# Kernel optimization log

Measured on AMD Instinct MI355X. Metric: run time of the kernel, lower is better.

Reference implementation:

```python
import jax, jax.numpy as jnp
import numpy as np

N_NODES = 131072      # total nodes across all graphs
IN_CHANNELS = 256     # node attribute dim after continuous WL embedding
NUM_PROJ = 256        # num_projections
NUM_QUANT = 256       # num_quantiles
NUM_GRAPHS = 256      # batch of graphs (equal-sized segments of 512 nodes)
P_NORM = 2            # p-sliced Wasserstein


def setup_inputs() -> dict:
    key = jax.random.key(0)
    k1, k2 = jax.random.split(key)
    x = jax.random.normal(k1, (N_NODES, IN_CHANNELS), dtype=jnp.float32)
    # fixed random projections, column-normalized (resample_projections)
    projections = jax.random.normal(k2, (IN_CHANNELS, NUM_PROJ), dtype=jnp.float32)
    projections = projections / jnp.sqrt(jnp.sum(projections ** 2, axis=0, keepdims=True))
    # cum_weights buffer: linspace(0, 1, num_quantiles)
    cum_weights = jnp.linspace(0.0, 1.0, NUM_QUANT, dtype=jnp.float32)
    # equal-sized graph segments (sorted segment ids), jit-friendly
    batch = (jnp.arange(N_NODES, dtype=jnp.int32) // (N_NODES // NUM_GRAPHS))
    return {
        "x": x,
        "projections": projections,
        "cum_weights": cum_weights,
        "batch": batch,
        "num_graphs": NUM_GRAPHS,
    }


def reference(x, projections, cum_weights, batch, num_graphs):
    # x: [N, C], projections: [C, P], cum_weights: [Q]
    n_nodes = x.shape[0]
    num_p = projections.shape[1]
    num_q = cum_weights.shape[0]
    nodes_per_graph = n_nodes // num_graphs

    xp = jnp.matmul(x, projections)                       # [N, P]
    xg = xp.reshape(num_graphs, nodes_per_graph, num_p)   # [B, n, P]
    xs = jnp.sort(xg, axis=1)                             # segmented sort per graph
    # torch.quantile(..., interpolation='lower'): index = floor(q * (n-1))
    idx = jnp.floor(cum_weights * (nodes_per_graph - 1)).astype(jnp.int32)  # [Q]
    quant = xs[:, idx, :]                                 # [B, Q, P]
    scale = (num_q * num_p) ** (1.0 / P_NORM)
    return quant.reshape(num_graphs, num_q * num_p) / scale
```

## Files before the change

kernel.cpp:

```cpp
#include <hip/hip_runtime.h>
#include <hip/hip_fp16.h>

typedef unsigned short u16;
typedef unsigned int u32;
typedef __bf16 bf16x8 __attribute__((ext_vector_type(8)));
typedef float f32x4 __attribute__((ext_vector_type(4)));


__device__ __forceinline__ u16 f2bf(float f) {
  union { float f; u32 u; } v; v.f = f;
  u32 r = (v.u + 0x7FFFu + ((v.u >> 16) & 1u)) >> 16;
  return (u16)r;
}

__device__ __forceinline__ u32 cvtpk(float a, float b) {
  u32 r; asm("v_cvt_pk_bf16_f32 %0, %1, %2" : "=v"(r) : "v"(a), "v"(b));
  return r;
}

__device__ __forceinline__ u32 pkh(float a, float b) {
  return (u32)__half_as_ushort(__float2half(a)) |
         ((u32)__half_as_ushort(__float2half(b)) << 16);
}

__device__ __forceinline__ u32 vperm(u32 s0, u32 s1, u32 sel) {
  u32 r; asm("v_perm_b32 %0, %1, %2, %3" : "=v"(r) : "v"(s0), "v"(s1), "s"(sel));
  return r;
}

__device__ __forceinline__ u32 pkmin(u32 a, u32 b) {
  u32 r; asm("v_pk_min_f16 %0, %1, %2" : "=v"(r) : "v"(a), "v"(b)); return r;
}
__device__ __forceinline__ u32 pkmax(u32 a, u32 b) {
  u32 r; asm("v_pk_max_f16 %0, %1, %2" : "=v"(r) : "v"(a), "v"(b)); return r;
}

template <int CTRL> __device__ __forceinline__ u32 xdpp(u32 x) {
  return (u32)__builtin_amdgcn_mov_dpp((int)x, CTRL, 0xF, 0xF, true);
}
template <int IMM> __device__ __forceinline__ u32 xswz(u32 x) {
  return (u32)__builtin_amdgcn_ds_swizzle((int)x, IMM);
}
#define EX_X1(x)  xdpp<0xB1>(x)
#define EX_X2(x)  xdpp<0x4E>(x)
#define EX_F3(x)  xdpp<0x1B>(x)
#define EX_F7(x)  xdpp<0x141>(x)
#define EX_F15(x) xdpp<0x140>(x)
#define EX_X8(x)  xdpp<0x128>(x)
#define EX_X4(x)  xswz<0x101F>(x)
#define EX_X16(x) xswz<0x401F>(x)
#define EX_F31(x) xswz<0x7C1F>(x)
#define EX_F63(x) ((u32)__shfl_xor((int)(x), 63, 64))

__global__ __launch_bounds__(256) void transpose_proj(const float* __restrict__ proj,
                                                      u16* __restrict__ projT) {
  const int k = blockIdx.x;
  const int p = threadIdx.x;
  projT[(size_t)p * 256 + k] = f2bf(proj[(size_t)k * 256 + p]);
}

__global__ __launch_bounds__(1024) void fused_swe(const float* __restrict__ x,
                                                  const u16* __restrict__ projT,
                                                  const float* __restrict__ cw,
                                                  float* __restrict__ out) {
  extern __shared__ __attribute__((aligned(16))) char lds[];
  u32* res = (u32*)(lds + 32768);

  const int tid = threadIdx.x;
  const int lane = tid & 63;
  const int w = tid >> 6;
  const int g = blockIdx.x;
  const int quad = lane >> 4;
  const int m16 = lane & 15;

  bf16x8 a[2][8];
#pragma unroll
  for (int t = 0; t < 2; ++t) {
    const float* ap = x + (size_t)(g * 512 + w * 32 + t * 16 + m16) * 256 + quad * 8;
#pragma unroll
    for (int ks = 0; ks < 8; ++ks) {
      float4 f0 = *(const float4*)(ap + ks * 32);
      float4 f1 = *(const float4*)(ap + ks * 32 + 4);
      u32 pk4[4] = { cvtpk(f0.x, f0.y), cvtpk(f0.z, f0.w),
                     cvtpk(f1.x, f1.y), cvtpk(f1.z, f1.w) };
      a[t][ks] = *(const bf16x8*)pk4;
    }
  }

  for (int qtr = 0; qtr < 4; ++qtr) {
    {
      const int row = tid >> 4;
      const int seg0 = tid & 15;
#pragma unroll
      for (int si = 0; si < 2; ++si) {
        const int seg = seg0 + si * 16;
        uint4 d = *(const uint4*)(projT + (size_t)(qtr * 64 + row) * 256 + seg * 8);
        *(uint4*)(lds + row * 512 + ((seg ^ (row & 7)) * 16)) = d;
      }
    }
    __syncthreads();

#pragma unroll
    for (int nt = 0; nt < 4; ++nt) {
      const int prow = nt * 16 + m16;
      const int rx = (prow & 7) << 4;
      const char* pb = lds + prow * 512;
      f32x4 acc0 = {0.f, 0.f, 0.f, 0.f};
      f32x4 acc1 = {0.f, 0.f, 0.f, 0.f};
#pragma unroll
      for (int ks = 0; ks < 8; ++ks) {
        bf16x8 bfrag = *(const bf16x8*)(pb + (((ks * 64) | (quad * 16)) ^ rx));
        acc0 = __builtin_amdgcn_mfma_f32_16x16x32_bf16(a[0][ks], bfrag, acc0, 0, 0, 0);
        acc1 = __builtin_amdgcn_mfma_f32_16x16x32_bf16(a[1][ks], bfrag, acc1, 0, 0, 0);
      }
      const int wb = prow * 260 + w * 16 + quad * 2;
      res[wb]     = pkh(acc0[0], acc0[1]);
      res[wb + 1] = pkh(acc0[2], acc0[3]);
      res[wb + 8] = pkh(acc1[0], acc1[1]);
      res[wb + 9] = pkh(acc1[2], acc1[3]);
    }
    __syncthreads();

#pragma unroll
    for (int s = 0; s < 2; ++s) {
      const int d = w * 2 + s;
      u32* ra = res + d * 260;
      u32* rb = res + (d + 32) * 260;
      uint4 a4 = *(const uint4*)(ra + lane * 4);
      uint4 b4 = *(const uint4*)(rb + lane * 4);
      u32 v[8];
      v[0] = vperm(b4.x, a4.x, 0x05040100u); v[1] = vperm(b4.x, a4.x, 0x07060302u);
      v[2] = vperm(b4.y, a4.y, 0x05040100u); v[3] = vperm(b4.y, a4.y, 0x07060302u);
      v[4] = vperm(b4.z, a4.z, 0x05040100u); v[5] = vperm(b4.z, a4.z, 0x07060302u);
      v[6] = vperm(b4.w, a4.w, 0x05040100u); v[7] = vperm(b4.w, a4.w, 0x07060302u);

#define CE(i, j) { u32 mn_ = pkmin(v[i], v[j]); u32 mx_ = pkmax(v[i], v[j]); v[i] = mn_; v[j] = mx_; }
#define INTRA3 \
  CE(0,4) CE(1,5) CE(2,6) CE(3,7) \
  CE(0,2) CE(1,3) CE(4,6) CE(5,7) \
  CE(0,1) CE(2,3) CE(4,5) CE(6,7)

#define FLIPP(EX, lowbit) { \
    const bool low_ = (lane & (lowbit)) == 0; \
    u32 t_[8]; \
    _Pragma("unroll") for (int r = 0; r < 8; ++r) t_[r] = EX(v[7 - r]); \
    _Pragma("unroll") for (int r = 0; r < 8; ++r) { \
      u32 mn_ = pkmin(v[r], t_[r]); u32 mx_ = pkmax(v[r], t_[r]); \
      v[r] = low_ ? mn_ : mx_; } }

#define XCROSSP(EX, lm) { \
    const bool low_ = (lane & (lm)) == 0; \
    _Pragma("unroll") for (int r = 0; r < 8; ++r) { \
      u32 t_ = EX(v[r]); \
      u32 mn_ = pkmin(v[r], t_); u32 mx_ = pkmax(v[r], t_); \
      v[r] = low_ ? mn_ : mx_; } }

      CE(0,1) CE(2,3) CE(4,5) CE(6,7)
      CE(0,3) CE(1,2) CE(4,7) CE(5,6)
      CE(0,1) CE(2,3) CE(4,5) CE(6,7)
      CE(0,7) CE(1,6) CE(2,5) CE(3,4)
      CE(0,2) CE(1,3) CE(4,6) CE(5,7)
      CE(0,1) CE(2,3) CE(4,5) CE(6,7)
      FLIPP(EX_X1, 1)  INTRA3
      FLIPP(EX_F3, 2)  XCROSSP(EX_X1, 1)  INTRA3
      FLIPP(EX_F7, 4)  XCROSSP(EX_X2, 2) XCROSSP(EX_X1, 1)  INTRA3
      FLIPP(EX_F15, 8) XCROSSP(EX_X4, 4) XCROSSP(EX_X2, 2) XCROSSP(EX_X1, 1)  INTRA3
      FLIPP(EX_F31, 16) XCROSSP(EX_X8, 8) XCROSSP(EX_X4, 4) XCROSSP(EX_X2, 2) XCROSSP(EX_X1, 1)  INTRA3
      FLIPP(EX_F63, 32) XCROSSP(EX_X16, 16) XCROSSP(EX_X8, 8) XCROSSP(EX_X4, 4) XCROSSP(EX_X2, 2) XCROSSP(EX_X1, 1)  INTRA3

#undef CE
#undef INTRA3
#undef FLIPP
#undef XCROSSP

      u32* pp = (lane < 32) ? (ra + lane * 8) : (rb + lane * 8 - 256);
      *(uint4*)pp       = (uint4){v[0], v[1], v[2], v[3]};
      *(uint4*)(pp + 4) = (uint4){v[4], v[5], v[6], v[7]};
    }
    __syncthreads();

#pragma unroll
    for (int it = 0; it < 16; ++it) {
      const int linear = it * 1024 + tid;
      const int q = linear >> 6;
      const int pc = linear & 63;
      const int iq = (int)floorf(cw[q] * 511.0f);
      const int dd = pc & 31;
      const u32 val = res[dd * 260 + ((iq >= 256) ? (iq + 8064) : iq)];
      const u16 h = (pc & 32) ? (u16)(val >> 16) : (u16)(val & 0xFFFF);
      __half_raw hr; hr.x = h;
      out[(size_t)g * 65536 + (size_t)q * 256 + qtr * 64 + pc] =
          __half2float(__half(hr)) * 0.00390625f;
    }
  }
}

extern "C" void kernel_launch(void* const* d_in, const int* in_sizes, int n_in,
                              void* d_out, int out_size, void* d_ws, size_t ws_size,
                              hipStream_t stream) {
  const float* x    = (const float*)d_in[0];
  const float* proj = (const float*)d_in[1];
  const float* cw   = (const float*)d_in[2];
  float* out = (float*)d_out;

  u16* projT = (u16*)d_ws;

  transpose_proj<<<256, 256, 0, stream>>>(proj, projT);
  fused_swe<<<256, 1024, 99328, stream>>>(x, projT, cw, out);
}
```

Baseline: 284.3 us.

## Split projections across two blocks per graph to double grid size

After: 398.6 us. +40.2%, slower.

```diff
diff --git a/kernel.cpp b/kernel.cpp
--- a/kernel.cpp
+++ b/kernel.cpp
@@ -59,17 +59,18 @@
   projT[(size_t)p * 256 + k] = f2bf(proj[(size_t)k * 256 + p]);
 }
 
-__global__ __launch_bounds__(1024) void fused_swe(const float* __restrict__ x,
-                                                  const u16* __restrict__ projT,
-                                                  const float* __restrict__ cw,
-                                                  float* __restrict__ out) {
+__global__ __launch_bounds__(1024, 8) void fused_swe(const float* __restrict__ x,
+                                                     const u16* __restrict__ projT,
+                                                     const float* __restrict__ cw,
+                                                     float* __restrict__ out) {
   extern __shared__ __attribute__((aligned(16))) char lds[];
-  u32* res = (u32*)(lds + 32768);
+  u32* res = (u32*)(lds + 16384);
 
   const int tid = threadIdx.x;
   const int lane = tid & 63;
   const int w = tid >> 6;
-  const int g = blockIdx.x;
+  const int g = blockIdx.x & 255;
+  const int h = blockIdx.x >> 8;
   const int quad = lane >> 4;
   const int m16 = lane & 15;
 
@@ -87,21 +88,19 @@
     }
   }
 
-  for (int qtr = 0; qtr < 4; ++qtr) {
+  for (int sl = 0; sl < 4; ++sl) {
+    const int pbase = h * 128 + sl * 32;
+
     {
-      const int row = tid >> 4;
-      const int seg0 = tid & 15;
-#pragma unroll
-      for (int si = 0; si < 2; ++si) {
-        const int seg = seg0 + si * 16;
-        uint4 d = *(const uint4*)(projT + (size_t)(qtr * 64 + row) * 256 + seg * 8);
-        *(uint4*)(lds + row * 512 + ((seg ^ (row & 7)) * 16)) = d;
-      }
+      const int row = tid >> 5;
+      const int seg = tid & 31;
+      uint4 d = *(const uint4*)(projT + (size_t)(pbase + row) * 256 + seg * 8);
+      *(uint4*)(lds + row * 512 + ((seg ^ (row & 7)) * 16)) = d;
     }
     __syncthreads();
 
 #pragma unroll
-    for (int nt = 0; nt < 4; ++nt) {
+    for (int nt = 0; nt < 2; ++nt) {
       const int prow = nt * 16 + m16;
       const int rx = (prow & 7) << 4;
       const char* pb = lds + prow * 512;
@@ -121,11 +120,9 @@
     }
     __syncthreads();
 
-#pragma unroll
-    for (int s = 0; s < 2; ++s) {
-      const int d = w * 2 + s;
-      u32* ra = res + d * 260;
-      u32* rb = res + (d + 32) * 260;
+    {
+      u32* ra = res + w * 260;
+      u32* rb = res + (w + 16) * 260;
       uint4 a4 = *(const uint4*)(ra + lane * 4);
       uint4 b4 = *(const uint4*)(rb + lane * 4);
       u32 v[8];
@@ -180,16 +177,16 @@
     __syncthreads();
 
 #pragma unroll
-    for (int it = 0; it < 16; ++it) {
+    for (int it = 0; it < 8; ++it) {
       const int linear = it * 1024 + tid;
-      const int q = linear >> 6;
-      const int pc = linear & 63;
+      const int q = linear >> 5;
+      const int pc = linear & 31;
       const int iq = (int)floorf(cw[q] * 511.0f);
-      const int dd = pc & 31;
-      const u32 val = res[dd * 260 + ((iq >= 256) ? (iq + 8064) : iq)];
-      const u16 h = (pc & 32) ? (u16)(val >> 16) : (u16)(val & 0xFFFF);
-      __half_raw hr; hr.x = h;
-      out[(size_t)g * 65536 + (size_t)q * 256 + qtr * 64 + pc] =
+      const int dd = pc & 15;
+      const u32 val = res[dd * 260 + ((iq >= 256) ? (iq + 3904) : iq)];
+      const u16 hh = (pc & 16) ? (u16)(val >> 16) : (u16)(val & 0xFFFF);
+      __half_raw hr; hr.x = hh;
+      out[(size_t)g * 65536 + (size_t)q * 256 + pbase + pc] =
           __half2float(__half(hr)) * 0.00390625f;
     }
   }
@@ -206,5 +203,5 @@
   u16* projT = (u16*)d_ws;
 
   transpose_proj<<<256, 256, 0, stream>>>(proj, projT);
-  fused_swe<<<256, 1024, 99328, stream>>>(x, projT, cw, out);
-}
+  fused_swe<<<512, 1024, 49664, stream>>>(x, projT, cw, out);
+}
```
